# Optimization experiments

Measured on AMD Instinct MI355X. Metric: run time of the kernel, lower is better.

## Reference

```python
import jax, jax.numpy as jnp
import numpy as np

N = 100000   # nodes
F = 128      # feature len
E = 1600000  # edges per graph (avg degree 16)


def setup_inputs() -> dict:
    key = jax.random.key(0)
    ks = jax.random.split(key, 32)
    def nrm(k, shape, scale=0.05):
        return jax.random.normal(k, shape, jnp.float32) * scale
    inp = {"X": jax.random.normal(ks[0], (N, F), jnp.float32)}
    i = 1
    for g in (1, 2, 3):
        inp[f"edge_index{g}"] = jax.random.randint(ks[i], (2, E), 0, N, dtype=jnp.int32); i += 1
        inp[f"edge_weight{g}"] = jax.random.uniform(ks[i], (E,), jnp.float32); i += 1
        inp[f"g{g}_w1"] = nrm(ks[i], (F, F)); i += 1
        inp[f"g{g}_b1"] = jnp.zeros((F,), jnp.float32)
        inp[f"g{g}_w2"] = nrm(ks[i], (F, F)); i += 1
        inp[f"g{g}_b2"] = jnp.zeros((F,), jnp.float32)
    for name in ("fc1", "fc2"):
        inp[f"{name}_w1"] = nrm(ks[i], (F, 256)); i += 1
        inp[f"{name}_b1"] = jnp.zeros((256,), jnp.float32)
        inp[f"{name}_w2"] = nrm(ks[i], (256, 128)); i += 1
        inp[f"{name}_b2"] = jnp.zeros((128,), jnp.float32)
        inp[f"{name}_w3"] = nrm(ks[i], (128, 64)); i += 1
        inp[f"{name}_b3"] = jnp.zeros((64,), jnp.float32)
    return inp


def gcn_conv(x, w, b, src, dst, ew):
    # PyG GCNConv: add self-loops (weight 1), symmetric normalization.
    n = x.shape[0]
    h = x @ w                                                   # [N, F]
    deg = jax.ops.segment_sum(ew, dst, num_segments=n) + 1.0    # [N]
    dinv = jax.lax.rsqrt(deg)
    norm = dinv[src] * ew * dinv[dst]                           # [E]
    agg = jax.ops.segment_sum(h[src] * norm[:, None], dst, num_segments=n)
    agg = agg + (dinv * dinv)[:, None] * h                      # self-loop term
    return agg + b


def single_module(x, src, dst, ew, w1, b1, w2, b2):
    x = jax.nn.relu(gcn_conv(x, w1, b1, src, dst, ew))
    x = jax.nn.relu(gcn_conv(x, w2, b2, src, dst, ew))
    return x


def fc_layer(x, w1, b1, w2, b2, w3, b3):
    x = jax.nn.relu(x @ w1 + b1)
    x = jax.nn.relu(x @ w2 + b2)
    return jax.nn.relu(x @ w3 + b3)


def reference(X, edge_index1, edge_weight1, g1_w1, g1_b1, g1_w2, g1_b2,
              edge_index2, edge_weight2, g2_w1, g2_b1, g2_w2, g2_b2,
              edge_index3, edge_weight3, g3_w1, g3_b1, g3_w2, g3_b2,
              fc1_w1, fc1_b1, fc1_w2, fc1_b2, fc1_w3, fc1_b3,
              fc2_w1, fc2_b1, fc2_w2, fc2_b2, fc2_w3, fc2_b3):
    X0 = fc_layer(X, fc1_w1, fc1_b1, fc1_w2, fc1_b2, fc1_w3, fc1_b3)
    X1 = single_module(X, edge_index1[0], edge_index1[1], edge_weight1, g1_w1, g1_b1, g1_w2, g1_b2)
    X1 = fc_layer(X1, fc2_w1, fc2_b1, fc2_w2, fc2_b2, fc2_w3, fc2_b3)
    X2 = single_module(X, edge_index2[0], edge_index2[1], edge_weight2, g2_w1, g2_b1, g2_w2, g2_b2)
    X2 = fc_layer(X2, fc2_w1, fc2_b1, fc2_w2, fc2_b2, fc2_w3, fc2_b3)
    X3 = single_module(X, edge_index3[0], edge_index3[1], edge_weight3, g3_w1, g3_b1, g3_w2, g3_b2)
    X3 = fc_layer(X3, fc2_w1, fc2_b1, fc2_w2, fc2_b2, fc2_w3, fc2_b3)
    Xs = X0 + X1 + X2 + X3
    return (Xs, X1, X2, X3)
```

## Files before the change

### kernel.cpp

```cpp
#include <hip/hip_runtime.h>


typedef short bf16x8 __attribute__((ext_vector_type(8)));
typedef float f32x4 __attribute__((ext_vector_type(4)));

#define BSHIFT 8
#define NBUCK_MAX 400
#define BCAP 6144
#define WDSCALE 8388608.f

static __device__ __forceinline__ float frelu(float x) { return x > 0.f ? x : 0.f; }

static __device__ __forceinline__ unsigned short f2bf(float f) {
    unsigned int u = __float_as_uint(f);
    u += 0x7fffu + ((u >> 16) & 1u);
    return (unsigned short)(u >> 16);
}
static __device__ __forceinline__ float bflo(unsigned int u) {
    return __uint_as_float(u << 16);
}
static __device__ __forceinline__ float bfhi(unsigned int u) {
    return __uint_as_float(u & 0xffff0000u);
}

__global__ void xconv(const float* __restrict__ src, unsigned short* __restrict__ dst, int n4) {
    int i = blockIdx.x * 256 + threadIdx.x;
    if (i >= n4) return;
    float4 v = *(const float4*)(src + (size_t)i * 4);
    ushort4 o = {f2bf(v.x), f2bf(v.y), f2bf(v.z), f2bf(v.w)};
    *(ushort4*)(dst + (size_t)i * 4) = o;
}

__global__ void wtrans(const float* __restrict__ src, unsigned short* __restrict__ dst,
                       int K, int M) {
    int i = blockIdx.x * 256 + threadIdx.x;
    if (i >= K * M) return;
    int m = i / K, k = i % K;
    dst[i] = f2bf(src[(size_t)k * M + m]);
}

__global__ void zero_small(int* __restrict__ p, int n) {
    int i = blockIdx.x * 256 + threadIdx.x;
    if (i < n) p[i] = 0;
}

__global__ __launch_bounds__(256) void part_k(
    const int* __restrict__ src, const int* __restrict__ dst,
    const float* __restrict__ ew, int* __restrict__ gcur,
    int2* __restrict__ part, int nE, int nbuck) {
    __shared__ int lh[4][NBUCK_MAX];
    __shared__ int gb[4][NBUCK_MAX];
    const int tid = threadIdx.x;
    const int w = tid >> 6;
    for (int t = tid; t < 4 * NBUCK_MAX; t += 256) ((int*)lh)[t] = 0;
    __syncthreads();
    const int e0 = blockIdx.x * 4096;
    int rk[16], bk[16];
#pragma unroll
    for (int j = 0; j < 16; ++j) {
        int e = e0 + j * 256 + tid;
        rk[j] = -1;
        if (e < nE) {
            int b = dst[e] >> BSHIFT;
            bk[j] = b;
            rk[j] = atomicAdd(&lh[w][b], 1);
        }
    }
    __syncthreads();
    for (int t = tid; t < nbuck; t += 256) {
        int c0 = lh[0][t], c1 = lh[1][t], c2 = lh[2][t], c3 = lh[3][t];
        int tot = c0 + c1 + c2 + c3;
        int base = tot ? atomicAdd(&gcur[t], tot) : 0;
        gb[0][t] = base;
        gb[1][t] = base + c0;
        gb[2][t] = base + c0 + c1;
        gb[3][t] = base + c0 + c1 + c2;
    }
    __syncthreads();
#pragma unroll
    for (int j = 0; j < 16; ++j) {
        int e = e0 + j * 256 + tid;
        if (e >= nE) continue;
        int b = bk[j];
        int slot = gb[w][b] + rk[j];
        if (slot >= 0 && slot < BCAP) {
            int s = src[e];
            int dl = dst[e] & ((1 << BSHIFT) - 1);
            part[(size_t)b * BCAP + slot] = make_int2(s | (dl << 17), __float_as_int(ew[e]));
        }
    }
}

__global__ void scanB(const int* __restrict__ gcur, int* __restrict__ bbase,
                      int* __restrict__ rp, int n, int nbuck) {
    __shared__ int s[512];
    int t = threadIdx.x;
    int c = (t < nbuck) ? gcur[t] : 0;
    if (c > BCAP) c = BCAP;
    s[t] = c;
    __syncthreads();
#pragma unroll
    for (int off = 1; off < 512; off <<= 1) {
        int x = (t >= off) ? s[t - off] : 0;
        __syncthreads();
        s[t] += x;
        __syncthreads();
    }
    if (t < nbuck) bbase[t] = s[t] - c;
    if (t == nbuck - 1) rp[n] = s[t];
}

__global__ __launch_bounds__(256) void csr_bucket(
    const int2* __restrict__ part, const int* __restrict__ gcur,
    const int* __restrict__ bbase, int2* __restrict__ ev,
    int* __restrict__ rp, float* __restrict__ dinv, int n) {
    __shared__ int hist[256];
    __shared__ int cur[256];
    __shared__ int wd[256];
    const int b = blockIdx.x;
    const int t = threadIdx.x;
    int cnt = gcur[b];
    if (cnt > BCAP) cnt = BCAP;
    const int gbase = bbase[b];
    const int2* pb = part + (size_t)b * BCAP;

    hist[t] = 0; wd[t] = 0;
    __syncthreads();
    for (int i = t; i < cnt; i += 256)
        atomicAdd(&hist[(pb[i].x >> 17) & 255], 1);
    __syncthreads();
    int myh = hist[t];
#pragma unroll
    for (int off = 1; off < 256; off <<= 1) {
        int x = (t >= off) ? hist[t - off] : 0;
        __syncthreads();
        hist[t] += x;
        __syncthreads();
    }
    int excl = hist[t] - myh;
    cur[t] = excl;
    __syncthreads();
    for (int i = t; i < cnt; i += 256) {
        int2 p = pb[i];
        int dl = (p.x >> 17) & 255;
        int pos = atomicAdd(&cur[dl], 1);
        ev[(size_t)gbase + pos] = make_int2(p.x & 0x1FFFF, p.y);
        atomicAdd(&wd[dl], (int)(__int_as_float(p.y) * WDSCALE + 0.5f));
    }
    __syncthreads();
    int g = (b << BSHIFT) + t;
    if (g < n) {
        dinv[g] = rsqrtf(1.f + (float)wd[t] * (1.f / WDSCALE));
        rp[g] = gbase + excl;
    }
}

__global__ __launch_bounds__(256) void gather_bf(
    const int* __restrict__ rp, const int2* __restrict__ ev,
    const unsigned short* __restrict__ h,
    const float* __restrict__ dinv, const float* __restrict__ bias,
    unsigned short* __restrict__ aggr, int n) {
    int node = (int)(((size_t)blockIdx.x * 256 + threadIdx.x) >> 6);
    if (node >= n) return;
    int lane = threadIdx.x & 63;
    float di = dinv[node];
    float sl = di * di;
    unsigned int hu = *(const unsigned int*)(h + (size_t)node * 128 + lane * 2);
    float2 bv = *(const float2*)(bias + lane * 2);
    float ax0 = 0.f, ay0 = 0.f, ax1 = 0.f, ay1 = 0.f;
    float ax2 = 0.f, ay2 = 0.f, ax3 = 0.f, ay3 = 0.f;
    const int beg = rp[node], end = rp[node + 1];
    int i = beg;
    for (; i + 7 < end; i += 8) {
        int2 e[8];
#pragma unroll
        for (int j = 0; j < 8; ++j) e[j] = ev[i + j];
        float nm[8];
#pragma unroll
        for (int j = 0; j < 8; ++j) nm[j] = dinv[e[j].x] * __int_as_float(e[j].y);
        unsigned int u[8];
#pragma unroll
        for (int j = 0; j < 8; ++j)
            u[j] = *(const unsigned int*)(h + (size_t)e[j].x * 128 + lane * 2);
        ax0 += nm[0] * bflo(u[0]); ay0 += nm[0] * bfhi(u[0]);
        ax1 += nm[1] * bflo(u[1]); ay1 += nm[1] * bfhi(u[1]);
        ax2 += nm[2] * bflo(u[2]); ay2 += nm[2] * bfhi(u[2]);
        ax3 += nm[3] * bflo(u[3]); ay3 += nm[3] * bfhi(u[3]);
        ax0 += nm[4] * bflo(u[4]); ay0 += nm[4] * bfhi(u[4]);
        ax1 += nm[5] * bflo(u[5]); ay1 += nm[5] * bfhi(u[5]);
        ax2 += nm[6] * bflo(u[6]); ay2 += nm[6] * bfhi(u[6]);
        ax3 += nm[7] * bflo(u[7]); ay3 += nm[7] * bfhi(u[7]);
    }
    for (; i + 3 < end; i += 4) {
        int2 e0 = ev[i], e1 = ev[i + 1], e2 = ev[i + 2], e3 = ev[i + 3];
        float n0 = dinv[e0.x] * __int_as_float(e0.y);
        float n1 = dinv[e1.x] * __int_as_float(e1.y);
        float n2 = dinv[e2.x] * __int_as_float(e2.y);
        float n3 = dinv[e3.x] * __int_as_float(e3.y);
        unsigned int u0 = *(const unsigned int*)(h + (size_t)e0.x * 128 + lane * 2);
        unsigned int u1 = *(const unsigned int*)(h + (size_t)e1.x * 128 + lane * 2);
        unsigned int u2 = *(const unsigned int*)(h + (size_t)e2.x * 128 + lane * 2);
        unsigned int u3 = *(const unsigned int*)(h + (size_t)e3.x * 128 + lane * 2);
        ax0 += n0 * bflo(u0); ay0 += n0 * bfhi(u0);
        ax1 += n1 * bflo(u1); ay1 += n1 * bfhi(u1);
        ax2 += n2 * bflo(u2); ay2 += n2 * bfhi(u2);
        ax3 += n3 * bflo(u3); ay3 += n3 * bfhi(u3);
    }
    for (; i < end; ++i) {
        int2 e0 = ev[i];
        float n0 = dinv[e0.x] * __int_as_float(e0.y);
        unsigned int u0 = *(const unsigned int*)(h + (size_t)e0.x * 128 + lane * 2);
        ax0 += n0 * bflo(u0); ay0 += n0 * bfhi(u0);
    }
    float ox = frelu(di * ((ax0 + ax1) + (ax2 + ax3)) + sl * bflo(hu) + bv.x);
    float oy = frelu(di * ((ay0 + ay1) + (ay2 + ay3)) + sl * bfhi(hu) + bv.y);
    unsigned int o = (unsigned int)f2bf(ox) | ((unsigned int)f2bf(oy) << 16);
    *(unsigned int*)(aggr + (size_t)node * 128 + lane * 2) = o;
}

template<int K, int BN, int RELU, int EPI>
__global__ __launch_bounds__(256, 2) void gemm_bf(
    const unsigned short* __restrict__ A, const unsigned short* __restrict__ Wt,
    const float* __restrict__ bias, void* __restrict__ Cout,
    int M, int nrows, float* __restrict__ xs) {
    constexpr int BM = 128, BK = 64;
    constexpr int WN = BN / 2;
    constexpr int NF = WN / 16;
    static_assert(BN == 64 || BN == 128, "BN");
    __shared__ unsigned short As[BM][BK + 8];
    __shared__ unsigned short Bs[BN][BK + 8];

    const int tid  = threadIdx.x;
    const int wid  = tid >> 6;
    const int lane = tid & 63;
    const int wm   = (wid >> 1) * 64;
    const int wn   = (wid & 1) * WN;
    const int row0 = blockIdx.x * BM;
    const int col0 = blockIdx.y * BN;
    const int lr   = lane & 15;
    const int lk   = (lane >> 4) * 8;

    f32x4 acc[4][NF] = {};

    for (int k0 = 0; k0 < K; k0 += BK) {
#pragma unroll
        for (int it = 0; it < 4; ++it) {
            int f = tid + it * 256;
            int r = f >> 3, g = f & 7;
            int grow = row0 + r;
            if (grow >= nrows) grow = nrows - 1;
            bf16x8 v = *(const bf16x8*)(A + (size_t)grow * K + k0 + g * 8);
            *(bf16x8*)&As[r][g * 8] = v;
        }
#pragma unroll
        for (int it = 0; it < BN / 32; ++it) {
            int f = tid + it * 256;
            int nidx = f >> 3, g = f & 7;
            bf16x8 v = *(const bf16x8*)(Wt + (size_t)(col0 + nidx) * K + k0 + g * 8);
            *(bf16x8*)&Bs[nidx][g * 8] = v;
        }
        __syncthreads();
#pragma unroll
        for (int kk = 0; kk < 2; ++kk) {
            bf16x8 af[4], bfv[NF];
#pragma unroll
            for (int mi = 0; mi < 4; ++mi)
                af[mi] = *(const bf16x8*)&As[wm + 16 * mi + lr][kk * 32 + lk];
#pragma unroll
            for (int ni = 0; ni < NF; ++ni)
                bfv[ni] = *(const bf16x8*)&Bs[wn + 16 * ni + lr][kk * 32 + lk];
#pragma unroll
            for (int mi = 0; mi < 4; ++mi)
#pragma unroll
                for (int ni = 0; ni < NF; ++ni)
                    acc[mi][ni] = __builtin_amdgcn_mfma_f32_16x16x32_bf16(
                        af[mi], bfv[ni], acc[mi][ni], 0, 0, 0);
        }
        __syncthreads();
    }

    const int dr0 = (lane >> 4) * 4;
#pragma unroll
    for (int ni = 0; ni < NF; ++ni) {
        int col = col0 + wn + 16 * ni + lr;
        float bv = bias ? bias[col] : 0.f;
#pragma unroll
        for (int mi = 0; mi < 4; ++mi) {
#pragma unroll
            for (int r = 0; r < 4; ++r) {
                int grow = row0 + wm + 16 * mi + dr0 + r;
                if (grow >= nrows) continue;
                float v = acc[mi][ni][r] + bv;
                if (RELU) v = frelu(v);
                if (EPI == 0) {
                    ((unsigned short*)Cout)[(size_t)grow * M + col] = f2bf(v);
                } else {
                    ((float*)Cout)[(size_t)grow * M + col] = v;
                    if (EPI == 2) xs[(size_t)grow * 64 + col] += v;
                }
            }
        }
    }
}

extern "C" void kernel_launch(void* const* d_in, const int* in_sizes, int n_in,
                              void* d_out, int out_size, void* d_ws, size_t ws_size,
                              hipStream_t stream) {
    (void)n_in; (void)out_size; (void)ws_size;
    const float* X = (const float*)d_in[0];
    const int N = in_sizes[0] / 128;

    const float* fc1_w1 = (const float*)d_in[19];
    const float* fc1_b1 = (const float*)d_in[20];
    const float* fc1_w2 = (const float*)d_in[21];
    const float* fc1_b2 = (const float*)d_in[22];
    const float* fc1_w3 = (const float*)d_in[23];
    const float* fc1_b3 = (const float*)d_in[24];
    const float* fc2_w1 = (const float*)d_in[25];
    const float* fc2_b1 = (const float*)d_in[26];
    const float* fc2_w2 = (const float*)d_in[27];
    const float* fc2_b2 = (const float*)d_in[28];
    const float* fc2_w3 = (const float*)d_in[29];
    const float* fc2_b3 = (const float*)d_in[30];

    float* out = (float*)d_out;
    float* Xs  = out;

    char* base = (char*)d_ws;
    const size_t Npad = (((size_t)N + 255) / 256) * 256;
    float*          dinv  = (float*)base;                 base += Npad * 4;
    unsigned short* Xbf   = (unsigned short*)base;        base += (size_t)N * 128 * 2;
    unsigned short* t1bf  = (unsigned short*)base;        base += (size_t)N * 256 * 2;
    unsigned short* t2bf  = (unsigned short*)base;        base += (size_t)N * 128 * 2;
    unsigned short* aggbf = (unsigned short*)base;        base += (size_t)N * 128 * 2;
    unsigned short* wtbuf = (unsigned short*)base;

    unsigned short* fc1w1t = wtbuf;
    unsigned short* fc1w2t = fc1w1t + 32768;
    unsigned short* fc1w3t = fc1w2t + 32768;
    unsigned short* fc2w1t = fc1w3t + 8192;
    unsigned short* fc2w2t = fc2w1t + 32768;
    unsigned short* fc2w3t = fc2w2t + 32768;
    unsigned short* gwt    = fc2w3t + 8192;

    const dim3 blk(256);
    const int GR = (N + 127) / 128;
    const int NBUCK = (N + 255) >> 8;
    const int GWB = (int)(((size_t)N * 64 + 255) / 256);

    xconv<<<(N * 32 + 255) / 256, blk, 0, stream>>>(X, Xbf, N * 32);
    wtrans<<<(128 * 256 + 255) / 256, blk, 0, stream>>>(fc1_w1, fc1w1t, 128, 256);
    wtrans<<<(256 * 128 + 255) / 256, blk, 0, stream>>>(fc1_w2, fc1w2t, 256, 128);
    wtrans<<<(128 * 64 + 255) / 256, blk, 0, stream>>>(fc1_w3, fc1w3t, 128, 64);
    wtrans<<<(128 * 256 + 255) / 256, blk, 0, stream>>>(fc2_w1, fc2w1t, 128, 256);
    wtrans<<<(256 * 128 + 255) / 256, blk, 0, stream>>>(fc2_w2, fc2w2t, 256, 128);
    wtrans<<<(128 * 64 + 255) / 256, blk, 0, stream>>>(fc2_w3, fc2w3t, 128, 64);
    for (int g = 0; g < 3; ++g) {
        wtrans<<<(128 * 128 + 255) / 256, blk, 0, stream>>>(
            (const float*)d_in[3 + 6 * g], gwt + g * 32768, 128, 128);
        wtrans<<<(128 * 128 + 255) / 256, blk, 0, stream>>>(
            (const float*)d_in[5 + 6 * g], gwt + g * 32768 + 16384, 128, 128);
    }

    gemm_bf<128, 128, 1, 0><<<dim3(GR, 2), blk, 0, stream>>>(Xbf, fc1w1t, fc1_b1, t1bf, 256, N, nullptr);
    gemm_bf<256, 128, 1, 0><<<dim3(GR, 1), blk, 0, stream>>>(t1bf, fc1w2t, fc1_b2, t2bf, 128, N, nullptr);
    gemm_bf<128, 64, 1, 1><<<dim3(GR, 1), blk, 0, stream>>>(t2bf, fc1w3t, fc1_b3, Xs, 64, N, nullptr);

    for (int g = 0; g < 3; ++g) {
        const int*   ei  = (const int*)d_in[1 + 6 * g];
        const int    E   = in_sizes[1 + 6 * g] / 2;
        const int*   srp = ei;
        const int*   dsp = ei + E;
        const float* ew  = (const float*)d_in[2 + 6 * g];
        const float* b1  = (const float*)d_in[4 + 6 * g];
        const float* b2  = (const float*)d_in[6 + 6 * g];
        unsigned short* w1t = gwt + g * 32768;
        unsigned short* w2t = w1t + 16384;

        int2* part  = (int2*)t1bf;
        int2* ev    = part + (size_t)NBUCK * BCAP;
        int*  rpn   = (int*)(ev + E);
        int*  gcur  = rpn + (N + 1);
        int*  bbase = gcur + NBUCK;

        zero_small<<<(NBUCK + 255) / 256, blk, 0, stream>>>(gcur, NBUCK);
        part_k<<<(E + 4095) / 4096, blk, 0, stream>>>(srp, dsp, ew, gcur, part, E, NBUCK);
        scanB<<<1, 512, 0, stream>>>(gcur, bbase, rpn, N, NBUCK);
        csr_bucket<<<NBUCK, blk, 0, stream>>>(part, gcur, bbase, ev, rpn, dinv, N);

        gemm_bf<128, 128, 0, 0><<<dim3(GR, 1), blk, 0, stream>>>(Xbf, w1t, nullptr, t2bf, 128, N, nullptr);
        gather_bf<<<GWB, blk, 0, stream>>>(rpn, ev, t2bf, dinv, b1, aggbf, N);
        gemm_bf<128, 128, 0, 0><<<dim3(GR, 1), blk, 0, stream>>>(aggbf, w2t, nullptr, t2bf, 128, N, nullptr);
        gather_bf<<<GWB, blk, 0, stream>>>(rpn, ev, t2bf, dinv, b2, aggbf, N);

        gemm_bf<128, 128, 1, 0><<<dim3(GR, 2), blk, 0, stream>>>(aggbf, fc2w1t, fc2_b1, t1bf, 256, N, nullptr);
        gemm_bf<256, 128, 1, 0><<<dim3(GR, 1), blk, 0, stream>>>(t1bf, fc2w2t, fc2_b2, t2bf, 128, N, nullptr);
        gemm_bf<128, 64, 1, 2><<<dim3(GR, 1), blk, 0, stream>>>(
            t2bf, fc2w3t, fc2_b3, out + (size_t)(1 + g) * N * 64, 64, N, Xs);
    }
}
```

Before: 1.099 ms.

## Fuse three-layer FC MLP into a single LDS-resident kernel

Replaces the three separate bf16 GEMM launches of each FC chain with one fused kernel. Each 128-row block loads its input tile once, computes the 256-wide hidden layer in 64-column chunks and consumes each chunk straight into the second layer's accumulators, then runs the third layer from shared memory. This removes the global-memory round-trips of the 256- and 128-wide intermediates, and two launches per chain. The cost is about 70 KB of LDS per block, which limits occupancy to 2 blocks per CU, plus extra barriers inside the chunk loop.

Result: faster. 970.8 us (-11.6%).

```diff
diff --git a/kernel.cpp b/kernel.cpp
--- a/kernel.cpp
+++ b/kernel.cpp
@@ -303,6 +303,155 @@
     }
 }
 
+template<int EPI>
+__global__ __launch_bounds__(256, 2) void fc_chain(
+    const unsigned short* __restrict__ A,
+    const unsigned short* __restrict__ W1t, const float* __restrict__ b1,
+    const unsigned short* __restrict__ W2t, const float* __restrict__ b2,
+    const unsigned short* __restrict__ W3t, const float* __restrict__ b3,
+    float* __restrict__ Cout, int nrows, float* __restrict__ xs) {
+    __shared__ unsigned short Ain[128 * 136];
+    __shared__ unsigned short T1q[128 * 72];
+    __shared__ unsigned short Bst[128 * 72];
+
+    const int tid  = threadIdx.x;
+    const int wid  = tid >> 6;
+    const int lane = tid & 63;
+    const int wm   = (wid >> 1) * 64;
+    const int wnH  = (wid & 1) * 32;
+    const int wnF  = (wid & 1) * 64;
+    const int row0 = blockIdx.x * 128;
+    const int lr   = lane & 15;
+    const int lk   = (lane >> 4) * 8;
+    const int dr0  = (lane >> 4) * 4;
+
+#pragma unroll
+    for (int it = 0; it < 8; ++it) {
+        int f = tid + it * 256;
+        int r = f >> 4, g = f & 15;
+        int grow = row0 + r; if (grow >= nrows) grow = nrows - 1;
+        *(bf16x8*)&Ain[r * 136 + g * 8] =
+            *(const bf16x8*)(A + (size_t)grow * 128 + g * 8);
+    }
+
+    f32x4 acc2[4][4] = {};
+
+    for (int q = 0; q < 4; ++q) {
+        __syncthreads();
+#pragma unroll
+        for (int it = 0; it < 4; ++it) {
+            int f = tid + it * 256;
+            int r = f >> 4, g = f & 15;
+            *(bf16x8*)&Bst[r * 136 + g * 8] =
+                *(const bf16x8*)(W1t + (size_t)(q * 64 + r) * 128 + g * 8);
+        }
+        __syncthreads();
+        f32x4 acc1[4][2] = {};
+#pragma unroll
+        for (int kk = 0; kk < 4; ++kk) {
+            bf16x8 af[4], bw[2];
+#pragma unroll
+            for (int mi = 0; mi < 4; ++mi)
+                af[mi] = *(const bf16x8*)&Ain[(wm + 16 * mi + lr) * 136 + kk * 32 + lk];
+#pragma unroll
+            for (int ni = 0; ni < 2; ++ni)
+                bw[ni] = *(const bf16x8*)&Bst[(wnH + 16 * ni + lr) * 136 + kk * 32 + lk];
+#pragma unroll
+            for (int mi = 0; mi < 4; ++mi)
+#pragma unroll
+                for (int ni = 0; ni < 2; ++ni)
+                    acc1[mi][ni] = __builtin_amdgcn_mfma_f32_16x16x32_bf16(
+                        af[mi], bw[ni], acc1[mi][ni], 0, 0, 0);
+        }
+        __syncthreads();
+#pragma unroll
+        for (int ni = 0; ni < 2; ++ni) {
+            float bv = b1[q * 64 + wnH + 16 * ni + lr];
+#pragma unroll
+            for (int mi = 0; mi < 4; ++mi)
+#pragma unroll
+                for (int r = 0; r < 4; ++r)
+                    T1q[(wm + 16 * mi + dr0 + r) * 72 + wnH + 16 * ni + lr] =
+                        f2bf(frelu(acc1[mi][ni][r] + bv));
+        }
+#pragma unroll
+        for (int it = 0; it < 4; ++it) {
+            int f = tid + it * 256;
+            int r = f >> 3, g = f & 7;
+            *(bf16x8*)&Bst[r * 72 + g * 8] =
+                *(const bf16x8*)(W2t + (size_t)r * 256 + q * 64 + g * 8);
+        }
+        __syncthreads();
+#pragma unroll
+        for (int kk = 0; kk < 2; ++kk) {
+            bf16x8 af[4], bw[4];
+#pragma unroll
+            for (int mi = 0; mi < 4; ++mi)
+                af[mi] = *(const bf16x8*)&T1q[(wm + 16 * mi + lr) * 72 + kk * 32 + lk];
+#pragma unroll
+            for (int ni = 0; ni < 4; ++ni)
+                bw[ni] = *(const bf16x8*)&Bst[(wnF + 16 * ni + lr) * 72 + kk * 32 + lk];
+#pragma unroll
+            for (int mi = 0; mi < 4; ++mi)
+#pragma unroll
+                for (int ni = 0; ni < 4; ++ni)
+                    acc2[mi][ni] = __builtin_amdgcn_mfma_f32_16x16x32_bf16(
+                        af[mi], bw[ni], acc2[mi][ni], 0, 0, 0);
+        }
+    }
+    __syncthreads();
+#pragma unroll
+    for (int ni = 0; ni < 4; ++ni) {
+        float bv = b2[wnF + 16 * ni + lr];
+#pragma unroll
+        for (int mi = 0; mi < 4; ++mi)
+#pragma unroll
+            for (int r = 0; r < 4; ++r)
+                Ain[(wm + 16 * mi + dr0 + r) * 136 + wnF + 16 * ni + lr] =
+                    f2bf(frelu(acc2[mi][ni][r] + bv));
+    }
+#pragma unroll
+    for (int it = 0; it < 4; ++it) {
+        int f = tid + it * 256;
+        int r = f >> 4, g = f & 15;
+        *(bf16x8*)&Bst[r * 136 + g * 8] =
+            *(const bf16x8*)(W3t + (size_t)r * 128 + g * 8);
+    }
+    __syncthreads();
+    f32x4 acc3[4][2] = {};
+#pragma unroll
+    for (int kk = 0; kk < 4; ++kk) {
+        bf16x8 af[4], bw[2];
+#pragma unroll
+        for (int mi = 0; mi < 4; ++mi)
+            af[mi] = *(const bf16x8*)&Ain[(wm + 16 * mi + lr) * 136 + kk * 32 + lk];
+#pragma unroll
+        for (int ni = 0; ni < 2; ++ni)
+            bw[ni] = *(const bf16x8*)&Bst[(wnH + 16 * ni + lr) * 136 + kk * 32 + lk];
+#pragma unroll
+        for (int mi = 0; mi < 4; ++mi)
+#pragma unroll
+            for (int ni = 0; ni < 2; ++ni)
+                acc3[mi][ni] = __builtin_amdgcn_mfma_f32_16x16x32_bf16(
+                    af[mi], bw[ni], acc3[mi][ni], 0, 0, 0);
+    }
+#pragma unroll
+    for (int ni = 0; ni < 2; ++ni) {
+        int col = wnH + 16 * ni + lr;
+        float bv = b3[col];
+#pragma unroll
+        for (int mi = 0; mi < 4; ++mi)
+#pragma unroll
+            for (int r = 0; r < 4; ++r) {
+                int grow = row0 + wm + 16 * mi + dr0 + r;
+                if (grow >= nrows) continue;
+                float v = frelu(acc3[mi][ni][r] + bv);
+                Cout[(size_t)grow * 64 + col] = v;
+                if (EPI == 2) xs[(size_t)grow * 64 + col] += v;
+            }
+    }
+}
+
 extern "C" void kernel_launch(void* const* d_in, const int* in_sizes, int n_in,
                               void* d_out, int out_size, void* d_ws, size_t ws_size,
                               hipStream_t stream) {
@@ -362,9 +511,8 @@
             (const float*)d_in[5 + 6 * g], gwt + g * 32768 + 16384, 128, 128);
     }
 
-    gemm_bf<128, 128, 1, 0><<<dim3(GR, 2), blk, 0, stream>>>(Xbf, fc1w1t, fc1_b1, t1bf, 256, N, nullptr);
-    gemm_bf<256, 128, 1, 0><<<dim3(GR, 1), blk, 0, stream>>>(t1bf, fc1w2t, fc1_b2, t2bf, 128, N, nullptr);
-    gemm_bf<128, 64, 1, 1><<<dim3(GR, 1), blk, 0, stream>>>(t2bf, fc1w3t, fc1_b3, Xs, 64, N, nullptr);
+    fc_chain<1><<<GR, blk, 0, stream>>>(Xbf, fc1w1t, fc1_b1, fc1w2t, fc1_b2,
+                                        fc1w3t, fc1_b3, Xs, N, nullptr);
 
     for (int g = 0; g < 3; ++g) {
         const int*   ei  = (const int*)d_in[1 + 6 * g];
@@ -393,9 +541,8 @@
         gemm_bf<128, 128, 0, 0><<<dim3(GR, 1), blk, 0, stream>>>(aggbf, w2t, nullptr, t2bf, 128, N, nullptr);
         gather_bf<<<GWB, blk, 0, stream>>>(rpn, ev, t2bf, dinv, b2, aggbf, N);
 
-        gemm_bf<128, 128, 1, 0><<<dim3(GR, 2), blk, 0, stream>>>(aggbf, fc2w1t, fc2_b1, t1bf, 256, N, nullptr);
-        gemm_bf<256, 128, 1, 0><<<dim3(GR, 1), blk, 0, stream>>>(t1bf, fc2w2t, fc2_b2, t2bf, 128, N, nullptr);
-        gemm_bf<128, 64, 1, 2><<<dim3(GR, 1), blk, 0, stream>>>(
-            t2bf, fc2w3t, fc2_b3, out + (size_t)(1 + g) * N * 64, 64, N, Xs);
-    }
-}
+        fc_chain<2><<<GR, blk, 0, stream>>>(aggbf, fc2w1t, fc2_b1, fc2w2t, fc2_b2,
+                                            fc2w3t, fc2_b3,
+                                            out + (size_t)(1 + g) * N * 64, N, Xs);
+    }
+}
```
